# Kernel optimization log

Measured on AMD Instinct MI355X. Metric: run time of the kernel, lower is better.

## Reference

```python
import jax, jax.numpy as jnp
import numpy as np
import math

B, N, D = 2, 4096, 1024
H, R, M = 16, 4, 8
BUCKET = 64

def setup_inputs() -> dict:
    key = jax.random.key(0)
    k1, k2, k3, k4, k5 = jax.random.split(key, 5)
    d = D // H
    return {
        "query": jax.random.normal(k1, (B, N, D), jnp.float32),
        "key": jax.random.normal(k2, (B, N, D), jnp.float32),
        "value": jax.random.normal(k3, (B, N, D), jnp.float32),
        "valence": jax.random.uniform(k4, (B,), jnp.float32),
        "hash_projections": jax.random.normal(k5, (R, H, d, M), jnp.float32),
        "valence_scale": jnp.ones((1,), jnp.float32),
    }

def reference(query, key, value, valence, hash_projections, valence_scale):
    b, n, dm = query.shape
    h = H
    d = dm // h
    r, _, _, m = hash_projections.shape
    c = n // BUCKET  # n_buckets (must divide exactly, matching torch view)
    # (B,N,D) -> (B,H,N,d)
    Q = query.reshape(b, n, h, d).transpose(0, 2, 1, 3)
    K = key.reshape(b, n, h, d).transpose(0, 2, 1, 3)
    V = value.reshape(b, n, h, d).transpose(0, 2, 1, 3)
    # LSH hash: argmax over M random projections per round -> (B,R,H,N)
    hashes = jnp.einsum('bhnd,rhdm->brhnm', Q, hash_projections)
    codes = jnp.argmax(hashes, axis=-1)
    # valence modulation (torch: scale.long().clamp(1, M); int truncation)
    scale = 1.0 + valence_scale[0] * valence.mean()
    scale_i = jnp.clip(scale.astype(jnp.int32), 1, m)
    codes = codes * scale_i
    # sort positions by hash code per (B,R,H)
    idx = jnp.argsort(codes, axis=-1)  # (B,R,H,N)
    idx_e = idx[..., None]  # (B,R,H,N,1), broadcasts over d
    K_sorted = jnp.take_along_axis(K[:, None], idx_e, axis=3)  # (B,R,H,N,d)
    V_sorted = jnp.take_along_axis(V[:, None], idx_e, axis=3)
    Kb = K_sorted.reshape(b, r, h, c, BUCKET, d)
    Vb = V_sorted.reshape(b, r, h, c, BUCKET, d)
    # NOTE: queries are bucketed in ORIGINAL order (faithful to source)
    Qb = Q.reshape(b, h, c, BUCKET, d)
    scores = jnp.einsum('bhcsd,brhced->brhcse', Qb, Kb) / math.sqrt(d)
    attn = jax.nn.softmax(scores, axis=-1)  # (B,R,H,C,S,E)
    outb = jnp.einsum('brhcse,brhced->brhcsd', attn, Vb)
    out = outb.reshape(b, r, h, n, d).mean(axis=1)  # average over hash rounds
    out = out.transpose(0, 2, 1, 3).reshape(b, n, dm)  # dropout is identity (eval)
    return out, attn.mean(axis=(1, 2))
```

## Files before the change

kernel.cpp:

```cpp
#include <hip/hip_runtime.h>
#include <hip/hip_bf16.h>

#define BB 2
#define NN 4096
#define DD 1024
#define HH 16
#define RR 4
#define MM 8
#define CC 64
#define DH 64
#define PAD 68

typedef __attribute__((ext_vector_type(8))) short bf16x8;
typedef __attribute__((ext_vector_type(8))) unsigned short ushort8;
typedef __attribute__((ext_vector_type(4))) float f32x4;
typedef unsigned long long u64;

__device__ __forceinline__ unsigned short f2bf(float x) {
  union { __hip_bfloat16 b; unsigned short u; } cv;
  cv.b = __float2bfloat16(x);
  return cv.u;
}
__device__ __forceinline__ int swz(int row, int colbyte) {
  return row * 128 + (colbyte ^ ((row & 7) << 4));
}
__device__ __forceinline__ bf16x8 pack8(float4 a, float4 b, float sc) {
  bf16x8 r;
  const float* pa = (const float*)&a;
  const float* pb = (const float*)&b;
#pragma unroll
  for (int j = 0; j < 4; ++j) {
    r[j] = (short)f2bf(pa[j] * sc);
    r[j + 4] = (short)f2bf(pb[j] * sc);
  }
  return r;
}

__global__ __launch_bounds__(256) void k_cvt(const float* __restrict__ kmat,
                                             const float* __restrict__ vmat,
                                             unsigned short* __restrict__ kbf,
                                             unsigned short* __restrict__ vbf) {
  int bid = blockIdx.x;
  int sel = bid >> 8;
  int rest = bid & 255;
  int b = rest >> 7;
  int chunk = rest & 127;
  const float* src = sel ? vmat : kmat;
  unsigned short* dst = sel ? vbf : kbf;
  int tid = threadIdx.x;
  int row = chunk * 32 + (tid >> 3), oct = tid & 7;
  const float* s0 = src + (size_t)(b * NN + row) * DD + oct * 8;
  unsigned short* d0 = dst + (size_t)b * HH * NN * 64 + (size_t)row * 64 + oct * 8;
#pragma unroll 4
  for (int h = 0; h < HH; ++h) {
    float4 a = *(const float4*)(s0 + h * 64);
    float4 c = *(const float4*)(s0 + h * 64 + 4);
    const float* af = (const float*)&a;
    const float* cf = (const float*)&c;
    ushort8 o;
#pragma unroll
    for (int j = 0; j < 4; ++j) {
      o[j] = f2bf(af[j]);
      o[j + 4] = f2bf(cf[j]);
    }
    *(ushort8*)(d0 + (size_t)h * NN * 64) = o;
  }
}

__global__ __launch_bounds__(256) void k_hash(const float* __restrict__ q,
                                              const float* __restrict__ proj,
                                              int* __restrict__ codes) {
  int blk = blockIdx.x;
  int nc = blk & (CC - 1);
  int h = (blk >> 6) & (HH - 1);
  int b = blk >> 10;
  __shared__ float Qs[64][PAD];
  __shared__ float Ps[DH][MM];
  __shared__ float Ss[64][9];
  int tid = threadIdx.x;
  const float* qbase = q + ((size_t)(b * NN + nc * 64) * DD + h * DH);
  for (int f = tid; f < 1024; f += 256) {
    int row = f >> 4, c4 = f & 15;
    *(float4*)&Qs[row][c4 * 4] = *(const float4*)(qbase + (size_t)row * DD + c4 * 4);
  }
  int nl = tid >> 3, m = tid & 7;
  for (int r = 0; r < RR; ++r) {
    const float* pbase = proj + (size_t)(r * HH + h) * DH * MM;
    for (int f = tid; f < DH * MM / 4; f += 256)
      ((float4*)Ps)[f] = ((const float4*)pbase)[f];
    __syncthreads();
    float s0 = 0.f, s1 = 0.f;
#pragma unroll
    for (int kk = 0; kk < DH; ++kk) {
      float p = Ps[kk][m];
      s0 += Qs[nl][kk] * p;
      s1 += Qs[nl + 32][kk] * p;
    }
    Ss[nl][m] = s0;
    Ss[nl + 32][m] = s1;
    __syncthreads();
    if (tid < 64) {
      float best = Ss[tid][0];
      int bm = 0;
#pragma unroll
      for (int mm = 1; mm < MM; ++mm) {
        float vv = Ss[tid][mm];
        if (vv > best) { best = vv; bm = mm; }
      }
      codes[(size_t)((b * RR + r) * HH + h) * NN + nc * 64 + tid] = bm;
    }
    __syncthreads();
  }
}

__global__ __launch_bounds__(256) void k_sort(const int* __restrict__ codes,
                                              int* __restrict__ idxo) {
  int gblk = blockIdx.x;
  const int* cg = codes + (size_t)gblk * NN;
  int* ig = idxo + (size_t)gblk * NN;
  int tid = threadIdx.x, lane = tid & 63, w = tid >> 6;
  __shared__ u64 wtot[4][2];
  int myc[16];
#pragma unroll
  for (int qd = 0; qd < 4; ++qd) {
    int4 t4 = ((const int4*)(cg + tid * 16))[qd];
    myc[qd * 4 + 0] = t4.x; myc[qd * 4 + 1] = t4.y;
    myc[qd * 4 + 2] = t4.z; myc[qd * 4 + 3] = t4.w;
  }
  u64 c01 = 0, c23 = 0;
#pragma unroll
  for (int i = 0; i < 16; ++i) {
    int k = myc[i];
    u64 one = 1ull << (16 * (k & 3));
    if (k < 4) c01 += one; else c23 += one;
  }
  u64 i01 = c01, i23 = c23;
#pragma unroll
  for (int d = 1; d < 64; d <<= 1) {
    u64 t0 = __shfl_up(i01, d);
    u64 t1 = __shfl_up(i23, d);
    if (lane >= d) { i01 += t0; i23 += t1; }
  }
  if (lane == 63) { wtot[w][0] = i01; wtot[w][1] = i23; }
  __syncthreads();
  u64 base01 = 0, base23 = 0, g01 = 0, g23 = 0;
#pragma unroll
  for (int ww = 0; ww < 4; ++ww) {
    u64 a = wtot[ww][0], bq = wtot[ww][1];
    if (ww < w) { base01 += a; base23 += bq; }
    g01 += a; g23 += bq;
  }
  u64 p01 = g01 + (g01 << 16); p01 += (p01 << 32);
  u64 p23 = g23 + (g23 << 16); p23 += (p23 << 32);
  u64 cb01 = p01 << 16;
  u64 tot01 = (p01 >> 48) & 0xffffull;
  u64 cb23 = (p23 << 16) + tot01 * 0x0001000100010001ull;
  u64 o01 = cb01 + base01 + (i01 - c01);
  u64 o23 = cb23 + base23 + (i23 - c23);
#pragma unroll
  for (int i = 0; i < 16; ++i) {
    int k = myc[i];
    int sh = 16 * (k & 3);
    int off;
    if (k < 4) { off = (int)((o01 >> sh) & 0xffffull); o01 += 1ull << sh; }
    else       { off = (int)((o23 >> sh) & 0xffffull); o23 += 1ull << sh; }
    ig[off] = tid * 16 + i;
  }
}

__global__ __launch_bounds__(256, 4) void k_attn(const float* __restrict__ q,
                                                 const unsigned short* __restrict__ kbf,
                                                 const unsigned short* __restrict__ vbf,
                                                 const int* __restrict__ idxs,
                                                 float* __restrict__ out,
                                                 float* __restrict__ attn_part,
                                                 float* __restrict__ attn_out,
                                                 int atomic_attn) {
  __shared__ __align__(16) char KB[8192];
  __shared__ __align__(16) char VT[8192];
  __shared__ __align__(16) char PL[8192];
  __shared__ int sidx[RR][64];

  int bid = blockIdx.x;
  int blk = (bid & 7) * 256 + (bid >> 3);
  int cblk = blk & 63;
  int h = (blk >> 6) & 15;
  int b = blk >> 10;
  int tid = threadIdx.x;
  int lane = tid & 63;
  int w = tid >> 6;
  int g = lane >> 4;
  int cl = lane & 15;
  int e2 = tid & 31, dg = (tid >> 5) & 7;

  sidx[tid >> 6][tid & 63] =
      idxs[(size_t)((b * RR + (tid >> 6)) * HH + h) * NN + cblk * 64 + (tid & 63)];

  const unsigned short* kp = kbf + (size_t)(b * HH + h) * NN * 64;
  const unsigned short* vp = vbf + (size_t)(b * HH + h) * NN * 64;

  const float* qrow = q + (size_t)(b * NN + cblk * 64 + 16 * w + cl) * DD + h * DH;
  bf16x8 qh[2];
#pragma unroll
  for (int ks = 0; ks < 2; ++ks)
    qh[ks] = pack8(*(const float4*)(qrow + 32 * ks + 8 * g),
                   *(const float4*)(qrow + 32 * ks + 8 * g + 4), 0.125f);

  __syncthreads();

  {
    const unsigned short* kr = kp + (size_t)sidx[0][16 * w + cl] * 64 + g * 8;
    ushort8 k0a = *(const ushort8*)kr;
    ushort8 k0b = *(const ushort8*)(kr + 32);
    ushort8 v0r = *(const ushort8*)(vp + (size_t)sidx[0][2 * e2] * 64 + dg * 8);
    ushort8 v1r = *(const ushort8*)(vp + (size_t)sidx[0][2 * e2 + 1] * 64 + dg * 8);
    *(ushort8*)(KB + w * 2048 + g * 256 + cl * 16) = k0a;
    *(ushort8*)(KB + w * 2048 + 1024 + g * 256 + cl * 16) = k0b;
#pragma unroll
    for (int j = 0; j < 8; ++j) {
      unsigned pk = (unsigned)(unsigned short)v0r[j] |
                    ((unsigned)(unsigned short)v1r[j] << 16);
      *(unsigned*)(VT + swz(8 * dg + j, 4 * e2)) = pk;
    }
  }
  __syncthreads();

  f32x4 acc_o[4];
  float attA[4][4];
#pragma unroll
  for (int t = 0; t < 4; ++t) {
    acc_o[t] = (f32x4){0.f, 0.f, 0.f, 0.f};
#pragma unroll
    for (int i = 0; i < 4; ++i) attA[t][i] = 0.f;
  }

#pragma unroll
  for (int r = 0; r < RR; ++r) {
    ushort8 kna, knb, n0r, n1r;
    if (r < RR - 1) {
      const unsigned short* krn = kp + (size_t)sidx[r + 1][16 * w + cl] * 64 + g * 8;
      kna = *(const ushort8*)krn;
      knb = *(const ushort8*)(krn + 32);
      n0r = *(const ushort8*)(vp + (size_t)sidx[r + 1][2 * e2] * 64 + dg * 8);
      n1r = *(const ushort8*)(vp + (size_t)sidx[r + 1][2 * e2 + 1] * 64 + dg * 8);
    }

    f32x4 s4[4];
#pragma unroll
    for (int t = 0; t < 4; ++t) s4[t] = (f32x4){0.f, 0.f, 0.f, 0.f};
    __builtin_amdgcn_s_setprio(1);
#pragma unroll
    for (int t = 0; t < 4; ++t)
#pragma unroll
      for (int ks = 0; ks < 2; ++ks) {
        bf16x8 kf = *(const bf16x8*)(KB + t * 2048 + ks * 1024 + g * 256 + cl * 16);
        s4[t] = __builtin_amdgcn_mfma_f32_16x16x32_bf16(kf, qh[ks], s4[t], 0, 0, 0);
      }
    __builtin_amdgcn_s_setprio(0);

    {
      f32x4 m4 = s4[0];
#pragma unroll
      for (int t = 1; t < 4; ++t)
#pragma unroll
        for (int i = 0; i < 4; ++i) m4[i] = fmaxf(m4[i], s4[t][i]);
      float mx = fmaxf(fmaxf(m4[0], m4[1]), fmaxf(m4[2], m4[3]));
      mx = fmaxf(mx, __shfl_xor(mx, 16));
      mx = fmaxf(mx, __shfl_xor(mx, 32));
      float sm = 0.f;
#pragma unroll
      for (int t = 0; t < 4; ++t)
#pragma unroll
        for (int i = 0; i < 4; ++i) {
          float e = __expf(s4[t][i] - mx);
          s4[t][i] = e;
          sm += e;
        }
      sm += __shfl_xor(sm, 16);
      sm += __shfl_xor(sm, 32);
      float inv = __builtin_amdgcn_rcpf(sm);
#pragma unroll
      for (int t = 0; t < 4; ++t)
#pragma unroll
        for (int i = 0; i < 4; ++i) {
          s4[t][i] *= inv;
          attA[t][i] += s4[t][i];
        }
    }

#pragma unroll
    for (int t = 0; t < 4; ++t) {
      u64 pk = (u64)f2bf(s4[t][0]) | ((u64)f2bf(s4[t][1]) << 16) |
               ((u64)f2bf(s4[t][2]) << 32) | ((u64)f2bf(s4[t][3]) << 48);
      *(u64*)(PL + w * 2048 + swz(cl, 32 * t + 8 * g)) = pk;
    }
    bf16x8 pa[2];
#pragma unroll
    for (int ks = 0; ks < 2; ++ks)
      pa[ks] = *(const bf16x8*)(PL + w * 2048 + swz(cl, 64 * ks + 16 * g));

    __builtin_amdgcn_s_setprio(1);
#pragma unroll
    for (int t = 0; t < 4; ++t)
#pragma unroll
      for (int ks = 0; ks < 2; ++ks) {
        bf16x8 vt = *(const bf16x8*)(VT + swz(16 * t + cl, ks * 64 + g * 16));
        acc_o[t] = __builtin_amdgcn_mfma_f32_16x16x32_bf16(vt, pa[ks], acc_o[t], 0, 0, 0);
      }
    __builtin_amdgcn_s_setprio(0);

    if (r < RR - 1) {
      __syncthreads();
      *(ushort8*)(KB + w * 2048 + g * 256 + cl * 16) = kna;
      *(ushort8*)(KB + w * 2048 + 1024 + g * 256 + cl * 16) = knb;
#pragma unroll
      for (int j = 0; j < 8; ++j) {
        unsigned pk = (unsigned)(unsigned short)n0r[j] |
                      ((unsigned)(unsigned short)n1r[j] << 16);
        *(unsigned*)(VT + swz(8 * dg + j, 4 * e2)) = pk;
      }
      __syncthreads();
    }
  }

  int srow = 16 * w + cl;
  size_t ob = (size_t)(b * NN + cblk * 64 + srow) * DD + h * DH + 4 * g;
#pragma unroll
  for (int t = 0; t < 4; ++t) {
    float4 o = make_float4(acc_o[t][0] * 0.25f, acc_o[t][1] * 0.25f,
                           acc_o[t][2] * 0.25f, acc_o[t][3] * 0.25f);
    *(float4*)(out + ob + 16 * t) = o;
  }
  size_t ab = (((size_t)(b * HH + h) * CC + cblk) * 64 + srow) * 64 + 4 * g;
  if (atomic_attn) {
    const float sc = 1.f / (RR * HH);
    size_t abase = (((size_t)b * CC + cblk) * 64 + srow) * 64 + 4 * g;
#pragma unroll
    for (int t = 0; t < 4; ++t)
#pragma unroll
      for (int i = 0; i < 4; ++i)
        atomicAdd(attn_out + abase + 16 * t + i, attA[t][i] * sc);
  } else {
#pragma unroll
    for (int t = 0; t < 4; ++t) {
      float4 o = make_float4(attA[t][0], attA[t][1], attA[t][2], attA[t][3]);
      *(float4*)(attn_part + ab + 16 * t) = o;
    }
  }
}

__global__ __launch_bounds__(256) void k_attn_reduce(const float* __restrict__ part,
                                                     float* __restrict__ attn_out) {
  size_t o = (size_t)blockIdx.x * 256 + threadIdx.x;
  int se = (int)(o & 4095);
  size_t bc = o >> 12;
  int c = (int)(bc & (CC - 1));
  int b = (int)(bc >> 6);
  float s = 0.f;
  const float* p = part + ((size_t)b * HH * CC + c) * 4096 + se;
#pragma unroll
  for (int h = 0; h < HH; ++h) s += p[(size_t)h * CC * 4096];
  attn_out[o] = s * (1.f / (RR * HH));
}

extern "C" void kernel_launch(void* const* d_in, const int* in_sizes, int n_in,
                              void* d_out, int out_size, void* d_ws, size_t ws_size,
                              hipStream_t stream) {
  const float* q = (const float*)d_in[0];
  const float* k = (const float*)d_in[1];
  const float* v = (const float*)d_in[2];
  const float* proj = (const float*)d_in[4];
  float* out = (float*)d_out;
  float* attn_out = out + (size_t)BB * NN * DD;

  const size_t n_codes = (size_t)BB * RR * HH * NN;
  const size_t n_panel = (size_t)BB * HH * NN * 64;
  const size_t n_part  = (size_t)BB * HH * CC * 4096;

  int* codes = (int*)d_ws;
  int* idxs = codes + n_codes;
  unsigned short* kbf = (unsigned short*)(idxs + n_codes);
  unsigned short* vbf = kbf + n_panel;
  float* attn_part = (float*)(vbf + n_panel);

  size_t need_full = n_codes * 8 + n_panel * 4 + n_part * 4;
  int atomic_attn = (ws_size < need_full) ? 1 : 0;
  if (atomic_attn)
    hipMemsetAsync(attn_out, 0, (size_t)BB * CC * 4096 * sizeof(float), stream);

  k_cvt<<<2 * BB * (NN / 32), 256, 0, stream>>>(k, v, kbf, vbf);
  k_hash<<<BB * HH * CC, 256, 0, stream>>>(q, proj, codes);
  k_sort<<<BB * RR * HH, 256, 0, stream>>>(codes, idxs);
  k_attn<<<BB * HH * CC, 256, 0, stream>>>(q, kbf, vbf, idxs, out, attn_part,
                                           attn_out, atomic_attn);
  if (!atomic_attn)
    k_attn_reduce<<<BB * CC * 4096 / 256, 256, 0, stream>>>(attn_part, attn_out);
}
```

Before: 93.17 us.

## Merge convert and hash kernels; store per-head attention partials in bf16

Folds the K/V bf16 conversion and the LSH hashing into one launch by giving the block index space to both jobs. The per-head attention-probability partials are now written and read as bf16 instead of fp32, which halves the traffic of the partial buffer (about 64 MB at fp32) between the attention and reduction kernels. This adds rounding error to the averaged attention output and lowers the workspace needed for the non-atomic path.

```diff
diff --git a/kernel.cpp b/kernel.cpp
--- a/kernel.cpp
+++ b/kernel.cpp
@@ -21,6 +21,9 @@
   cv.b = __float2bfloat16(x);
   return cv.u;
 }
+__device__ __forceinline__ float bf2f(unsigned short s) {
+  return __uint_as_float(((unsigned)s) << 16);
+}
 __device__ __forceinline__ int swz(int row, int colbyte) {
   return row * 128 + (colbyte ^ ((row & 7) << 4));
 }
@@ -36,48 +39,50 @@
   return r;
 }
 
-__global__ __launch_bounds__(256) void k_cvt(const float* __restrict__ kmat,
-                                             const float* __restrict__ vmat,
-                                             unsigned short* __restrict__ kbf,
-                                             unsigned short* __restrict__ vbf) {
+__global__ __launch_bounds__(256) void k_prep(const float* __restrict__ kmat,
+                                              const float* __restrict__ vmat,
+                                              const float* __restrict__ q,
+                                              const float* __restrict__ proj,
+                                              unsigned short* __restrict__ kbf,
+                                              unsigned short* __restrict__ vbf,
+                                              int* __restrict__ codes) {
+  __shared__ float Qs[64][PAD];
+  __shared__ float Ps[DH][MM];
+  __shared__ float Ss[64][9];
   int bid = blockIdx.x;
-  int sel = bid >> 8;
-  int rest = bid & 255;
-  int b = rest >> 7;
-  int chunk = rest & 127;
-  const float* src = sel ? vmat : kmat;
-  unsigned short* dst = sel ? vbf : kbf;
   int tid = threadIdx.x;
-  int row = chunk * 32 + (tid >> 3), oct = tid & 7;
-  const float* s0 = src + (size_t)(b * NN + row) * DD + oct * 8;
-  unsigned short* d0 = dst + (size_t)b * HH * NN * 64 + (size_t)row * 64 + oct * 8;
+
+  if (bid < 512) {
+    int sel = bid >> 8;
+    int rest = bid & 255;
+    int b = rest >> 7;
+    int chunk = rest & 127;
+    const float* src = sel ? vmat : kmat;
+    unsigned short* dst = sel ? vbf : kbf;
+    int row = chunk * 32 + (tid >> 3), oct = tid & 7;
+    const float* s0 = src + (size_t)(b * NN + row) * DD + oct * 8;
+    unsigned short* d0 = dst + (size_t)b * HH * NN * 64 + (size_t)row * 64 + oct * 8;
 #pragma unroll 4
-  for (int h = 0; h < HH; ++h) {
-    float4 a = *(const float4*)(s0 + h * 64);
-    float4 c = *(const float4*)(s0 + h * 64 + 4);
-    const float* af = (const float*)&a;
-    const float* cf = (const float*)&c;
-    ushort8 o;
-#pragma unroll
-    for (int j = 0; j < 4; ++j) {
-      o[j] = f2bf(af[j]);
-      o[j + 4] = f2bf(cf[j]);
-    }
-    *(ushort8*)(d0 + (size_t)h * NN * 64) = o;
-  }
-}
-
-__global__ __launch_bounds__(256) void k_hash(const float* __restrict__ q,
-                                              const float* __restrict__ proj,
-                                              int* __restrict__ codes) {
-  int blk = blockIdx.x;
+    for (int h = 0; h < HH; ++h) {
+      float4 a = *(const float4*)(s0 + h * 64);
+      float4 c = *(const float4*)(s0 + h * 64 + 4);
+      const float* af = (const float*)&a;
+      const float* cf = (const float*)&c;
+      ushort8 o;
+#pragma unroll
+      for (int j = 0; j < 4; ++j) {
+        o[j] = f2bf(af[j]);
+        o[j + 4] = f2bf(cf[j]);
+      }
+      *(ushort8*)(d0 + (size_t)h * NN * 64) = o;
+    }
+    return;
+  }
+
+  int blk = bid - 512;
   int nc = blk & (CC - 1);
   int h = (blk >> 6) & (HH - 1);
   int b = blk >> 10;
-  __shared__ float Qs[64][PAD];
-  __shared__ float Ps[DH][MM];
-  __shared__ float Ss[64][9];
-  int tid = threadIdx.x;
   const float* qbase = q + ((size_t)(b * NN + nc * 64) * DD + h * DH);
   for (int f = tid; f < 1024; f += 256) {
     int row = f >> 4, c4 = f & 15;
@@ -173,7 +178,7 @@
                                                  const unsigned short* __restrict__ vbf,
                                                  const int* __restrict__ idxs,
                                                  float* __restrict__ out,
-                                                 float* __restrict__ attn_part,
+                                                 unsigned short* __restrict__ attn_part,
                                                  float* __restrict__ attn_out,
                                                  int atomic_attn) {
   __shared__ __align__(16) char KB[8192];
@@ -331,7 +336,6 @@
                            acc_o[t][2] * 0.25f, acc_o[t][3] * 0.25f);
     *(float4*)(out + ob + 16 * t) = o;
   }
-  size_t ab = (((size_t)(b * HH + h) * CC + cblk) * 64 + srow) * 64 + 4 * g;
   if (atomic_attn) {
     const float sc = 1.f / (RR * HH);
     size_t abase = (((size_t)b * CC + cblk) * 64 + srow) * 64 + 4 * g;
@@ -341,15 +345,18 @@
       for (int i = 0; i < 4; ++i)
         atomicAdd(attn_out + abase + 16 * t + i, attA[t][i] * sc);
   } else {
+    unsigned short* ap =
+        attn_part + (((size_t)(b * HH + h) * CC + cblk) * 64 + srow) * 64 + 4 * g;
 #pragma unroll
     for (int t = 0; t < 4; ++t) {
-      float4 o = make_float4(attA[t][0], attA[t][1], attA[t][2], attA[t][3]);
-      *(float4*)(attn_part + ab + 16 * t) = o;
-    }
-  }
-}
-
-__global__ __launch_bounds__(256) void k_attn_reduce(const float* __restrict__ part,
+      u64 pk = (u64)f2bf(attA[t][0]) | ((u64)f2bf(attA[t][1]) << 16) |
+               ((u64)f2bf(attA[t][2]) << 32) | ((u64)f2bf(attA[t][3]) << 48);
+      *(u64*)(ap + 16 * t) = pk;
+    }
+  }
+}
+
+__global__ __launch_bounds__(256) void k_attn_reduce(const unsigned short* __restrict__ part,
                                                      float* __restrict__ attn_out) {
   size_t o = (size_t)blockIdx.x * 256 + threadIdx.x;
   int se = (int)(o & 4095);
@@ -357,9 +364,9 @@
   int c = (int)(bc & (CC - 1));
   int b = (int)(bc >> 6);
   float s = 0.f;
-  const float* p = part + ((size_t)b * HH * CC + c) * 4096 + se;
-#pragma unroll
-  for (int h = 0; h < HH; ++h) s += p[(size_t)h * CC * 4096];
+  const unsigned short* p = part + ((size_t)b * HH * CC + c) * 4096 + se;
+#pragma unroll
+  for (int h = 0; h < HH; ++h) s += bf2f(p[(size_t)h * CC * 4096]);
   attn_out[o] = s * (1.f / (RR * HH));
 }
 
@@ -381,15 +388,14 @@
   int* idxs = codes + n_codes;
   unsigned short* kbf = (unsigned short*)(idxs + n_codes);
   unsigned short* vbf = kbf + n_panel;
-  float* attn_part = (float*)(vbf + n_panel);
-
-  size_t need_full = n_codes * 8 + n_panel * 4 + n_part * 4;
+  unsigned short* attn_part = vbf + n_panel;
+
+  size_t need_full = n_codes * 8 + n_panel * 4 + n_part * 2;
   int atomic_attn = (ws_size < need_full) ? 1 : 0;
   if (atomic_attn)
     hipMemsetAsync(attn_out, 0, (size_t)BB * CC * 4096 * sizeof(float), stream);
 
-  k_cvt<<<2 * BB * (NN / 32), 256, 0, stream>>>(k, v, kbf, vbf);
-  k_hash<<<BB * HH * CC, 256, 0, stream>>>(q, proj, codes);
+  k_prep<<<512 + BB * HH * CC, 256, 0, stream>>>(k, v, q, proj, kbf, vbf, codes);
   k_sort<<<BB * RR * HH, 256, 0, stream>>>(codes, idxs);
   k_attn<<<BB * HH * CC, 256, 0, stream>>>(q, kbf, vbf, idxs, out, attn_part,
                                            attn_out, atomic_attn);
```

New measurement: 87.78 us. 5.8% less time.
